# Kernel tuning notes

Hardware: AMD Instinct MI355X
Metric: run time of the kernel (lower is better)

Reference implementation:

```python
import jax, jax.numpy as jnp
import numpy as np
from jax import lax

B, N, C = 8, 1024, 768
H = 12          # num_heads
D = C // H      # head_dim = 64
CH = 2          # c_h head-mix group size
G = H // CH     # number of head groups = 6
CQ = CK = 3     # conv kernel sizes


def setup_inputs() -> dict:
    key = jax.random.key(0)
    ks = jax.random.split(key, 13)
    s = 0.02
    return {
        "query": jax.random.normal(ks[0], (B, N, C), jnp.float32),
        "key": jax.random.normal(ks[1], (B, N, C), jnp.float32),
        "value": jax.random.normal(ks[2], (B, N, C), jnp.float32),
        "Wq": jax.random.normal(ks[3], (C, C), jnp.float32) * s,
        "bq": jax.random.normal(ks[4], (C,), jnp.float32) * s,
        "Wk": jax.random.normal(ks[5], (C, C), jnp.float32) * s,
        "bk": jax.random.normal(ks[6], (C,), jnp.float32) * s,
        "Wv": jax.random.normal(ks[7], (C, C), jnp.float32) * s,
        "bv": jax.random.normal(ks[8], (C,), jnp.float32) * s,
        "conv_w": jax.random.normal(ks[9], (H, 1, CQ, CK), jnp.float32) * 0.2,  # depthwise OIHW
        "head_mix": jax.random.normal(ks[10], (G, CH, CH), jnp.float32) * 0.5
                    + jnp.broadcast_to(jnp.eye(CH, dtype=jnp.float32), (G, CH, CH)),
        "Wo": jax.random.normal(ks[11], (C, C), jnp.float32) * s,
        "bo": jax.random.normal(ks[12], (C,), jnp.float32) * s,
    }


def reference(query, key, value, Wq, bq, Wk, bk, Wv, bv, conv_w, head_mix, Wo, bo):
    # projections (torch Linear: x @ W.T + b), then split heads -> (B, H, N, D)
    Q = (query @ Wq.T + bq).reshape(B, N, H, D).transpose(0, 2, 1, 3)
    K = (key   @ Wk.T + bk).reshape(B, N, H, D).transpose(0, 2, 1, 3)
    V = (value @ Wv.T + bv).reshape(B, N, H, D).transpose(0, 2, 1, 3)

    # scores: (B, H, Nq, Nk)
    scores = jnp.einsum('bhqd,bhkd->bhqk', Q, K) / jnp.sqrt(jnp.float32(D))

    # depthwise conv over the (Nq, Nk) score plane, groups = num_heads
    conv_attn = lax.conv_general_dilated(
        scores, conv_w,
        window_strides=(1, 1),
        padding=((CQ // 2, CQ // 2), (CK // 2, CK // 2)),
        dimension_numbers=('NCHW', 'OIHW', 'NCHW'),
        feature_group_count=H,
    )

    attn = jax.nn.softmax(conv_attn, axis=-1)  # (B, H, Nq, Nk)

    # cross-head mixing within groups of c_h heads
    attn_g = attn.reshape(B, G, CH, N, N)
    mixed = jnp.einsum('bghij,ghk->bgkij', attn_g, head_mix).reshape(B, H, N, N)

    out = jnp.einsum('bhqk,bhkd->bhqd', mixed, V)          # (B, H, N, D)
    out = out.transpose(0, 2, 1, 3).reshape(B, N, C)       # merge heads
    return out @ Wo.T + bo
```

## Files before the change

### kernel.cpp

```cpp
#include <hip/hip_runtime.h>
#include <stdint.h>

#define B_ 8
#define N_ 1024
#define C_ 768
#define H_ 12
#define G_ 6
#define QBLK 64
#define KSTEP 64
#define NQT 16
#define NKS 16

typedef __attribute__((ext_vector_type(8))) short bf16x8;
typedef __attribute__((ext_vector_type(8))) unsigned short u16x8;
typedef __attribute__((ext_vector_type(4))) float f32x4;

__device__ __forceinline__ float bf2f(unsigned short u) {
  return __uint_as_float(((unsigned)u) << 16);
}
__device__ __forceinline__ unsigned short f2bf(float f) {
  __bf16 b = (__bf16)f;
  unsigned short u;
  __builtin_memcpy(&u, &b, 2);
  return u;
}
__device__ __forceinline__ void gload16(const void* g, void* l) {
  __builtin_amdgcn_global_load_lds(
      (const __attribute__((address_space(1))) unsigned int*)g,
      (__attribute__((address_space(3))) unsigned int*)l, 16, 0, 0);
}

__global__ __launch_bounds__(256) void cvtX(
    const float* __restrict__ q, const float* __restrict__ k,
    const float* __restrict__ v, unsigned short* __restrict__ dst) {
  const float* src = (blockIdx.y == 0) ? q : (blockIdx.y == 1) ? k : v;
  unsigned short* d = dst + (size_t)blockIdx.y * ((size_t)B_ * N_ * C_);
  const size_t idx = ((size_t)blockIdx.x * 256 + threadIdx.x) * 8;
  const float4 f0 = *(const float4*)(src + idx);
  const float4 f1 = *(const float4*)(src + idx + 4);
  u16x8 o;
  o[0] = f2bf(f0.x); o[1] = f2bf(f0.y); o[2] = f2bf(f0.z); o[3] = f2bf(f0.w);
  o[4] = f2bf(f1.x); o[5] = f2bf(f1.y); o[6] = f2bf(f1.z); o[7] = f2bf(f1.w);
  *(u16x8*)(d + idx) = o;
}

__global__ __launch_bounds__(256) void cvtW(
    const float* __restrict__ wq, const float* __restrict__ wk,
    const float* __restrict__ wv, const float* __restrict__ wo,
    unsigned short* __restrict__ dst) {
  const float* src = (blockIdx.y == 0)   ? wq
                     : (blockIdx.y == 1) ? wk
                     : (blockIdx.y == 2) ? wv
                                         : wo;
  unsigned short* d = dst + (size_t)blockIdx.y * ((size_t)C_ * C_);
  const size_t idx = ((size_t)blockIdx.x * 256 + threadIdx.x) * 8;
  const float4 f0 = *(const float4*)(src + idx);
  const float4 f1 = *(const float4*)(src + idx + 4);
  u16x8 o;
  o[0] = f2bf(f0.x); o[1] = f2bf(f0.y); o[2] = f2bf(f0.z); o[3] = f2bf(f0.w);
  o[4] = f2bf(f1.x); o[5] = f2bf(f1.y); o[6] = f2bf(f1.z); o[7] = f2bf(f1.w);
  *(u16x8*)(d + idx) = o;
}

template <int MODE>
__device__ __forceinline__ void gemm_bf16(
    const unsigned short* __restrict__ X, const unsigned short* __restrict__ W,
    const float* __restrict__ bias, void* __restrict__ out, int row0, int col0,
    unsigned short* __restrict__ As, unsigned short* __restrict__ Bs) {
  const int tid = threadIdx.x;
  const int wid = tid >> 6, lane = tid & 63;
  const int lr = lane & 15, lk = (lane >> 4) << 3;
  const int qrow = (lane >> 4) << 2;
  const int wr = (wid & 1) << 6, wc = (wid >> 1) << 6;
  const int srow = (wid << 4) + (lane >> 2);
  const int scol = (lane & 3) << 3;
  const unsigned short* gA0 = X + (size_t)(row0 + srow) * C_ + scol;
  const unsigned short* gA1 = X + (size_t)(row0 + 64 + srow) * C_ + scol;
  const unsigned short* gB0 = W + (size_t)(col0 + srow) * C_ + scol;
  const unsigned short* gB1 = W + (size_t)(col0 + 64 + srow) * C_ + scol;
  unsigned short* lA0 = As + (wid << 9);
  unsigned short* lA1 = As + 2048 + (wid << 9);
  unsigned short* lB0 = Bs + (wid << 9);
  unsigned short* lB1 = Bs + 2048 + (wid << 9);
  f32x4 acc[4][4] = {};
  for (int k0 = 0; k0 < C_; k0 += 32) {
    gload16(gA0 + k0, lA0);
    gload16(gA1 + k0, lA1);
    gload16(gB0 + k0, lB0);
    gload16(gB1 + k0, lB1);
    __syncthreads();
    bf16x8 af[4], bg[4];
#pragma unroll
    for (int m = 0; m < 4; ++m)
      af[m] = *(const bf16x8*)&As[(wr + (m << 4) + lr) * 32 + lk];
#pragma unroll
    for (int n = 0; n < 4; ++n)
      bg[n] = *(const bf16x8*)&Bs[(wc + (n << 4) + lr) * 32 + lk];
#pragma unroll
    for (int m = 0; m < 4; ++m)
#pragma unroll
      for (int n = 0; n < 4; ++n)
        acc[m][n] = __builtin_amdgcn_mfma_f32_16x16x32_bf16(af[m], bg[n],
                                                            acc[m][n], 0, 0, 0);
    __syncthreads();
  }
#pragma unroll
  for (int m = 0; m < 4; ++m) {
#pragma unroll
    for (int n = 0; n < 4; ++n) {
      const int colc = col0 + wc + (n << 4) + lr;
      const float bv = bias[colc];
      if (MODE == 2) {
        const int r0 = row0 + wr + (m << 4) + qrow;
        const int bb = r0 >> 10, nn0 = r0 & 1023;
        const int hh = colc >> 6, dd = colc & 63;
        ushort4 pk;
        pk.x = f2bf(acc[m][n][0] + bv);
        pk.y = f2bf(acc[m][n][1] + bv);
        pk.z = f2bf(acc[m][n][2] + bv);
        pk.w = f2bf(acc[m][n][3] + bv);
        *(ushort4*)&((unsigned short*)out)[(((size_t)(bb * H_ + hh) << 6) + dd)
                                               * 1024 + nn0] = pk;
      } else {
#pragma unroll
        for (int q = 0; q < 4; ++q) {
          const int r = row0 + wr + (m << 4) + qrow + q;
          const float v = acc[m][n][q] + bv;
          if (MODE == 0) {
            ((float*)out)[(size_t)r * C_ + colc] = v;
          } else {
            const int bb = r >> 10, nn = r & 1023;
            const int hh = colc >> 6, dd = colc & 63;
            ((unsigned short*)out)[(((size_t)(bb * H_ + hh) << 10) + nn) * 64 +
                                   dd] = f2bf(v);
          }
        }
      }
    }
  }
}

__global__ __launch_bounds__(256) void proj3(
    const unsigned short* __restrict__ Xb, const unsigned short* __restrict__ Wb,
    const float* __restrict__ bq, const float* __restrict__ bk,
    const float* __restrict__ bv, unsigned short* Qb, unsigned short* Kb,
    unsigned short* Vt) {
  __shared__ __align__(16) unsigned short As[128 * 32];
  __shared__ __align__(16) unsigned short Bs[128 * 32];
  const int wg = blockIdx.x;
  const int nid = (wg & 7) * 144 + (wg >> 3);
  const int x = nid % 6, y = (nid / 6) & 63, z = nid / 384;
  const unsigned short* X = Xb + (size_t)z * B_ * N_ * C_;
  const unsigned short* W = Wb + (size_t)z * C_ * C_;
  if (z == 0)
    gemm_bf16<1>(X, W, bq, Qb, y << 7, x << 7, As, Bs);
  else if (z == 1)
    gemm_bf16<1>(X, W, bk, Kb, y << 7, x << 7, As, Bs);
  else
    gemm_bf16<2>(X, W, bv, Vt, y << 7, x << 7, As, Bs);
}

__global__ __launch_bounds__(256) void oproj(
    const unsigned short* __restrict__ X, const unsigned short* __restrict__ Wb,
    const float* __restrict__ bo, float* __restrict__ out) {
  __shared__ __align__(16) unsigned short As[128 * 32];
  __shared__ __align__(16) unsigned short Bs[128 * 32];
  const int wg = blockIdx.x;
  const int nid = (wg & 7) * 48 + (wg >> 3);
  const int x = nid % 6, y = nid / 6;
  gemm_bf16<0>(X, Wb + (size_t)3 * C_ * C_, bo, out, y << 7, x << 7, As, Bs);
}

__global__ __launch_bounds__(256, 2) void fused_attn(
    const unsigned short* __restrict__ Qb, const unsigned short* __restrict__ Kb,
    const unsigned short* __restrict__ Vt, const float* __restrict__ cw,
    const float* __restrict__ hm, unsigned short* __restrict__ pvout) {
  __shared__ __align__(16) unsigned char smem[52800];
  unsigned short* QPt = (unsigned short*)(smem + 33280);
  float* lsum = (float*)(smem + 52288);
#define KBASE(hh) (smem + (size_t)(hh)*8448)
#define VBASE(hh) (smem + 16896 + (size_t)(hh)*8192)

  const int wg = blockIdx.x;
  const int nid = (wg & 7) * 96 + (wg >> 3);
  const int qt = nid & 15;
  const int bg = nid >> 4;
  const int g = bg % G_, bb = bg / G_;
  const int i0 = qt << 6;

  const int tid = threadIdx.x;
  const int wid = tid >> 6, lane = tid & 63;
  const int lr = lane & 15, lg = lane >> 4;
  const int lk = lg << 3;

  const int h = wid >> 1, mt = wid & 1;

  const size_t HSTR = (size_t)N_ * 64;
  const unsigned short* Qz = Qb + (size_t)(bb * H_ + 2 * g) * HSTR;
  const unsigned short* Kz = Kb + (size_t)(bb * H_ + 2 * g) * HSTR;
  const unsigned short* Vz = Vt + (size_t)(bb * H_ + 2 * g) * HSTR;

  const int krow = tid >> 2, kd0 = (tid & 3) << 4;
  const int kc0 = (tid & 3) << 1;
  const int k2r = 64 + (tid >> 3), k2d = (tid & 7) << 3;
  const int vd = tid >> 2, vc0 = (tid & 3) << 4;

  u16x8 kreg[4], vreg[4];
  u16x8 kreg2[2];

  {
    const int gj = -1 + krow;
#pragma unroll
    for (int hh = 0; hh < 2; ++hh) {
      u16x8 a = {}, b = {};
      if (gj >= 0) {
        a = *(const u16x8*)(Kz + hh * HSTR + (size_t)gj * 64 + kd0);
        b = *(const u16x8*)(Kz + hh * HSTR + (size_t)gj * 64 + kd0 + 8);
      }
      kreg[2 * hh] = a; kreg[2 * hh + 1] = b;
    }
    if (tid < 16) {
      const int gj2 = -1 + k2r;
#pragma unroll
      for (int hh = 0; hh < 2; ++hh)
        kreg2[hh] = *(const u16x8*)(Kz + hh * HSTR + (size_t)gj2 * 64 + k2d);
    }
#pragma unroll
    for (int hh = 0; hh < 2; ++hh)
#pragma unroll
      for (int hf = 0; hf < 2; ++hf)
        vreg[2 * hh + hf] =
            *(const u16x8*)(Vz + hh * HSTR + (size_t)vd * 1024 + vc0 + (hf << 3));
  }

  {
    const int r = tid >> 2, d0 = (tid & 3) << 4;
    const int gi = i0 - 1 + r;
#pragma unroll
    for (int hh = 0; hh < 2; ++hh) {
      u16x8 qa = {}, qb = {};
      if (gi >= 0 && gi < N_) {
        qa = *(const u16x8*)(Qz + hh * HSTR + (size_t)gi * 64 + d0);
        qb = *(const u16x8*)(Qz + hh * HSTR + (size_t)gi * 64 + d0 + 8);
      }
      *(u16x8*)&QPt[((size_t)(hh * 66 + r)) * 72 + d0] = qa;
      *(u16x8*)&QPt[((size_t)(hh * 66 + r)) * 72 + d0 + 8] = qb;
    }
    if (tid < 16) {
      const int r2 = 64 + (tid >> 3);
      const int d0h = (tid & 7) << 3;
      const int gi2 = i0 - 1 + r2;
#pragma unroll
      for (int hh = 0; hh < 2; ++hh) {
        u16x8 qv = {};
        if (gi2 < N_)
          qv = *(const u16x8*)(Qz + hh * HSTR + (size_t)gi2 * 64 + d0h);
        *(u16x8*)&QPt[((size_t)(hh * 66 + r2)) * 72 + d0h] = qv;
      }
    }
  }
  __syncthreads();

  bf16x8 qtf[2][3][2];
  {
    float wc3[3][3];
#pragma unroll
    for (int a = 0; a < 3; ++a)
#pragma unroll
      for (int c = 0; c < 3; ++c)
        wc3[a][c] = cw[(2 * g + h) * 9 + a * 3 + c] *
                    (0.125f * 1.4426950408889634f);
#pragma unroll
    for (int qs = 0; qs < 2; ++qs) {
      const int ribase = (mt << 5) + (qs << 4) + lr;
#pragma unroll
      for (int dh = 0; dh < 2; ++dh) {
        const u16x8 qa =
            *(const u16x8*)&QPt[((size_t)(h * 66 + ribase + 0)) * 72 +
                                (dh << 5) + lk];
        const u16x8 qb =
            *(const u16x8*)&QPt[((size_t)(h * 66 + ribase + 1)) * 72 +
                                (dh << 5) + lk];
        const u16x8 qc =
            *(const u16x8*)&QPt[((size_t)(h * 66 + ribase + 2)) * 72 +
                                (dh << 5) + lk];
#pragma unroll
        for (int c = 0; c < 3; ++c) {
#pragma unroll
          for (int e = 0; e < 8; ++e) {
            const float v = bf2f(qa[e]) * wc3[0][c] + bf2f(qb[e]) * wc3[1][c] +
                            bf2f(qc[e]) * wc3[2][c];
            qtf[qs][c][dh][e] = (short)f2bf(v);
          }
        }
      }
    }
  }

  unsigned short* PtW = &QPt[(size_t)wid * 2304];

  const unsigned char* kbB = KBASE(h) + lr * 128;
  int kofs[3][2];
#pragma unroll
  for (int c = 0; c < 3; ++c)
#pragma unroll
    for (int dh = 0; dh < 2; ++dh)
      kofs[c][dh] = (((((dh << 2) + lg) ^ ((lr + c) & 7)) << 4)) + c * 128;
  const unsigned char* vbB0 = VBASE(0) + lr * 128;
  const unsigned char* vbB1 = VBASE(1) + lr * 128;
  int vofs[2];
#pragma unroll
  for (int kj = 0; kj < 2; ++kj)
    vofs[kj] = ((((kj << 2) + lg) ^ (lr & 7)) << 4);

  float mreg[2] = {-3.0e38f, -3.0e38f};
  float lreg[2] = {0.f, 0.f};
  f32x4 acc[2][2][4] = {};

  for (int s = 0; s < NKS; ++s) {
    {
      unsigned char* kr0 = KBASE(0) + krow * 128;
      unsigned char* kr1 = KBASE(1) + krow * 128;
      const int ksw = krow & 7;
      *(u16x8*)(kr0 + ((kc0 ^ ksw) << 4)) = kreg[0];
      *(u16x8*)(kr0 + (((kc0 + 1) ^ ksw) << 4)) = kreg[1];
      *(u16x8*)(kr1 + ((kc0 ^ ksw) << 4)) = kreg[2];
      *(u16x8*)(kr1 + (((kc0 + 1) ^ ksw) << 4)) = kreg[3];
      if (tid < 16) {
        const int k2sw = k2r & 7, k2c = tid & 7;
        *(u16x8*)(KBASE(0) + k2r * 128 + ((k2c ^ k2sw) << 4)) = kreg2[0];
        *(u16x8*)(KBASE(1) + k2r * 128 + ((k2c ^ k2sw) << 4)) = kreg2[1];
      }
      unsigned char* vr0 = VBASE(0) + vd * 128;
      unsigned char* vr1 = VBASE(1) + vd * 128;
      const int vsw = vd & 7, vcc = (tid & 3) << 1;
      *(u16x8*)(vr0 + ((vcc ^ vsw) << 4)) = vreg[0];
      *(u16x8*)(vr0 + (((vcc + 1) ^ vsw) << 4)) = vreg[1];
      *(u16x8*)(vr1 + ((vcc ^ vsw) << 4)) = vreg[2];
      *(u16x8*)(vr1 + (((vcc + 1) ^ vsw) << 4)) = vreg[3];
    }
    __syncthreads();

    if (s + 1 < NKS) {
      const int j1 = (s + 1) << 6;
      const int gj = j1 - 1 + krow;
#pragma unroll
      for (int hh = 0; hh < 2; ++hh) {
        kreg[2 * hh] = *(const u16x8*)(Kz + hh * HSTR + (size_t)gj * 64 + kd0);
        kreg[2 * hh + 1] =
            *(const u16x8*)(Kz + hh * HSTR + (size_t)gj * 64 + kd0 + 8);
      }
      if (tid < 16) {
        const int gj2 = j1 - 1 + k2r;
#pragma unroll
        for (int hh = 0; hh < 2; ++hh) {
          u16x8 a = {};
          if (gj2 < N_)
            a = *(const u16x8*)(Kz + hh * HSTR + (size_t)gj2 * 64 + k2d);
          kreg2[hh] = a;
        }
      }
#pragma unroll
      for (int hh = 0; hh < 2; ++hh)
#pragma unroll
        for (int hf = 0; hf < 2; ++hf)
          vreg[2 * hh + hf] = *(const u16x8*)(Vz + hh * HSTR + (size_t)vd * 1024 +
                                              j1 + vc0 + (hf << 3));
    }

    f32x4 racc[2][4] = {};
    __builtin_amdgcn_s_setprio(1);
#pragma unroll
    for (int c = 0; c < 3; ++c) {
#pragma unroll
      for (int dh = 0; dh < 2; ++dh) {
#pragma unroll
        for (int nt = 0; nt < 4; ++nt) {
          const bf16x8 ak = *(const bf16x8*)(kbB + nt * 2048 + kofs[c][dh]);
          racc[0][nt] = __builtin_amdgcn_mfma_f32_16x16x32_bf16(
              ak, qtf[0][c][dh], racc[0][nt], 0, 0, 0);
          racc[1][nt] = __builtin_amdgcn_mfma_f32_16x16x32_bf16(
              ak, qtf[1][c][dh], racc[1][nt], 0, 0, 0);
        }
      }
    }
    __builtin_amdgcn_s_setprio(0);

    {
      float pmax[2];
#pragma unroll
      for (int qs = 0; qs < 2; ++qs) {
        float pm = fmaxf(fmaxf(racc[qs][0][0], racc[qs][0][1]),
                         fmaxf(racc[qs][0][2], racc[qs][0][3]));
#pragma unroll
        for (int nt = 1; nt < 4; ++nt)
          pm = fmaxf(pm, fmaxf(fmaxf(racc[qs][nt][0], racc[qs][nt][1]),
                               fmaxf(racc[qs][nt][2], racc[qs][nt][3])));
        pm = fmaxf(pm, __shfl_xor(pm, 16));
        pm = fmaxf(pm, __shfl_xor(pm, 32));
        pmax[qs] = pm;
      }
      if (__any((pmax[0] > mreg[0] + 8.f) || (pmax[1] > mreg[1] + 8.f))) {
#pragma unroll
        for (int qs = 0; qs < 2; ++qs) {
          const float mn = fmaxf(mreg[qs], pmax[qs]);
          const float alpha = exp2f(mreg[qs] - mn);
          mreg[qs] = mn;
          lreg[qs] *= alpha;
          float a4[4];
#pragma unroll
          for (int q = 0; q < 4; ++q)
            a4[q] = __shfl(alpha, (lg << 4) | ((lg << 2) + q));
#pragma unroll
          for (int k2 = 0; k2 < 2; ++k2)
#pragma unroll
            for (int nt = 0; nt < 4; ++nt)
#pragma unroll
              for (int q = 0; q < 4; ++q) acc[k2][qs][nt][q] *= a4[q];
        }
      }
#pragma unroll
      for (int qs = 0; qs < 2; ++qs) {
        float rs = 0.f;
#pragma unroll
        for (int nt = 0; nt < 4; ++nt)
#pragma unroll
          for (int q = 0; q < 4; ++q) {
            const float p = exp2f(racc[qs][nt][q] - mreg[qs]);
            racc[qs][nt][q] = p;
            rs += p;
          }
        rs += __shfl_xor(rs, 16);
        rs += __shfl_xor(rs, 32);
        lreg[qs] += rs;
#pragma unroll
        for (int nt = 0; nt < 4; ++nt) {
          ushort4 pw;
          pw.x = f2bf(racc[qs][nt][0]); pw.y = f2bf(racc[qs][nt][1]);
          pw.z = f2bf(racc[qs][nt][2]); pw.w = f2bf(racc[qs][nt][3]);
          *(ushort4*)&PtW[(size_t)qs * 1152 + (size_t)lr * 72 + (nt << 4) +
                          (lg << 2)] = pw;
        }
      }
    }

    {
      bf16x8 paf[2][2];
#pragma unroll
      for (int qs = 0; qs < 2; ++qs) {
        paf[qs][0] = *(const bf16x8*)&PtW[(size_t)qs * 1152 + (size_t)lr * 72 + lk];
        paf[qs][1] =
            *(const bf16x8*)&PtW[(size_t)qs * 1152 + (size_t)lr * 72 + 32 + lk];
      }
      __builtin_amdgcn_s_setprio(1);
#pragma unroll
      for (int kj = 0; kj < 2; ++kj)
#pragma unroll
        for (int nt = 0; nt < 4; ++nt) {
          const bf16x8 bva = *(const bf16x8*)(vbB0 + nt * 2048 + vofs[kj]);
          const bf16x8 bvb = *(const bf16x8*)(vbB1 + nt * 2048 + vofs[kj]);
#pragma unroll
          for (int qs = 0; qs < 2; ++qs) {
            acc[0][qs][nt] = __builtin_amdgcn_mfma_f32_16x16x32_bf16(
                paf[qs][kj], bva, acc[0][qs][nt], 0, 0, 0);
            acc[1][qs][nt] = __builtin_amdgcn_mfma_f32_16x16x32_bf16(
                paf[qs][kj], bvb, acc[1][qs][nt], 0, 0, 0);
          }
        }
      __builtin_amdgcn_s_setprio(0);
    }
    __syncthreads();
  }

  if (lg == 0) {
    lsum[h * 64 + (mt << 5) + lr] = lreg[0];
    lsum[h * 64 + (mt << 5) + 16 + lr] = lreg[1];
  }
  __syncthreads();

  const float mw0 = hm[(g * 2 + h) * 2 + 0];
  const float mw1 = hm[(g * 2 + h) * 2 + 1];
  float* Os = (float*)smem;
  if (h == 1) {
#pragma unroll
    for (int qs = 0; qs < 2; ++qs)
#pragma unroll
      for (int q = 0; q < 4; ++q) {
        const int row = (mt << 5) + (qs << 4) + (lg << 2) + q;
        const float f0 = mw0 / lsum[64 + row];
        const float f1 = mw1 / lsum[64 + row];
#pragma unroll
        for (int nt = 0; nt < 4; ++nt) {
          Os[(size_t)(0 * 64 + row) * 68 + (nt << 4) + lr] =
              acc[0][qs][nt][q] * f0;
          Os[(size_t)(1 * 64 + row) * 68 + (nt << 4) + lr] =
              acc[1][qs][nt][q] * f1;
        }
      }
  }
  __syncthreads();
  if (h == 0) {
#pragma unroll
    for (int qs = 0; qs < 2; ++qs)
#pragma unroll
      for (int q = 0; q < 4; ++q) {
        const int row = (mt << 5) + (qs << 4) + (lg << 2) + q;
        const int gi = i0 + row;
        const float f0 = mw0 / lsum[row];
        const float f1 = mw1 / lsum[row];
#pragma unroll
        for (int nt = 0; nt < 4; ++nt) {
          const float v0 = acc[0][qs][nt][q] * f0 +
                           Os[(size_t)(0 * 64 + row) * 68 + (nt << 4) + lr];
          const float v1 = acc[1][qs][nt][q] * f1 +
                           Os[(size_t)(1 * 64 + row) * 68 + (nt << 4) + lr];
          pvout[(size_t)(bb * N_ + gi) * C_ + (2 * g + 0) * 64 + (nt << 4) +
                lr] = f2bf(v0);
          pvout[(size_t)(bb * N_ + gi) * C_ + (2 * g + 1) * 64 + (nt << 4) +
                lr] = f2bf(v1);
        }
      }
  }
#undef KBASE
#undef VBASE
}

extern "C" void kernel_launch(void* const* d_in, const int* in_sizes, int n_in,
                              void* d_out, int out_size, void* d_ws, size_t ws_size,
                              hipStream_t stream) {
  const float* query = (const float*)d_in[0];
  const float* key   = (const float*)d_in[1];
  const float* value = (const float*)d_in[2];
  const float* Wq = (const float*)d_in[3];
  const float* bq = (const float*)d_in[4];
  const float* Wk = (const float*)d_in[5];
  const float* bk = (const float*)d_in[6];
  const float* Wv = (const float*)d_in[7];
  const float* bv = (const float*)d_in[8];
  const float* cw = (const float*)d_in[9];
  const float* hm = (const float*)d_in[10];
  const float* Wo = (const float*)d_in[11];
  const float* bo = (const float*)d_in[12];
  float* out = (float*)d_out;

  char* ws = (char*)d_ws;
  const size_t SZ_BF = (size_t)B_ * H_ * N_ * 64 * 2;
  unsigned short* Qb = (unsigned short*)ws;
  unsigned short* Kb = (unsigned short*)(ws + SZ_BF);
  unsigned short* Vt = (unsigned short*)(ws + 2 * SZ_BF);
  unsigned short* pvb = (unsigned short*)(ws + 3 * SZ_BF);
  unsigned short* Xb = (unsigned short*)(ws + 4 * SZ_BF);
  unsigned short* Wb = (unsigned short*)(ws + 7 * SZ_BF);

  const dim3 blk(256);
  cvtX<<<dim3(3072, 3), blk, 0, stream>>>(query, key, value, Xb);
  cvtW<<<dim3(288, 4), blk, 0, stream>>>(Wq, Wk, Wv, Wo, Wb);
  proj3<<<dim3(1152), blk, 0, stream>>>(Xb, Wb, bq, bk, bv, Qb, Kb, Vt);
  fused_attn<<<dim3(768), blk, 0, stream>>>(Qb, Kb, Vt, cw, hm, pvb);
  oproj<<<dim3(384), blk, 0, stream>>>(pvb, Wb, bo, out);
}
```

Before: 177.6 us.

## Merge conversion kernels, load Q rows directly, and shrink attention LDS footprint

Merges the two fp32-to-bf16 conversion kernels into one launch. In the attention kernel, the Q halo rows are read straight from global memory into registers, which removes the Q LDS staging buffer and one barrier. The P-tile scratch is reduced to a single 16-row slab per wave by doing the P·V MFMAs immediately after each q-subtile's softmax. Together these cut shared memory from about 52.8 KB to 43 KB, which could allow more resident blocks, at the cost of redundant global reads of overlapping Q rows and less batching of the PV MFMAs.

Result: slower. 203.6 us (+14.7%).

```diff
diff --git a/kernel.cpp b/kernel.cpp
--- a/kernel.cpp
+++ b/kernel.cpp
@@ -30,30 +30,28 @@
       (__attribute__((address_space(3))) unsigned int*)l, 16, 0, 0);
 }
 
-__global__ __launch_bounds__(256) void cvtX(
+__global__ __launch_bounds__(256) void cvtAll(
     const float* __restrict__ q, const float* __restrict__ k,
-    const float* __restrict__ v, unsigned short* __restrict__ dst) {
-  const float* src = (blockIdx.y == 0) ? q : (blockIdx.y == 1) ? k : v;
-  unsigned short* d = dst + (size_t)blockIdx.y * ((size_t)B_ * N_ * C_);
-  const size_t idx = ((size_t)blockIdx.x * 256 + threadIdx.x) * 8;
-  const float4 f0 = *(const float4*)(src + idx);
-  const float4 f1 = *(const float4*)(src + idx + 4);
-  u16x8 o;
-  o[0] = f2bf(f0.x); o[1] = f2bf(f0.y); o[2] = f2bf(f0.z); o[3] = f2bf(f0.w);
-  o[4] = f2bf(f1.x); o[5] = f2bf(f1.y); o[6] = f2bf(f1.z); o[7] = f2bf(f1.w);
-  *(u16x8*)(d + idx) = o;
-}
-
-__global__ __launch_bounds__(256) void cvtW(
-    const float* __restrict__ wq, const float* __restrict__ wk,
-    const float* __restrict__ wv, const float* __restrict__ wo,
-    unsigned short* __restrict__ dst) {
-  const float* src = (blockIdx.y == 0)   ? wq
-                     : (blockIdx.y == 1) ? wk
-                     : (blockIdx.y == 2) ? wv
-                                         : wo;
-  unsigned short* d = dst + (size_t)blockIdx.y * ((size_t)C_ * C_);
-  const size_t idx = ((size_t)blockIdx.x * 256 + threadIdx.x) * 8;
+    const float* __restrict__ v, const float* __restrict__ wq,
+    const float* __restrict__ wk, const float* __restrict__ wv,
+    const float* __restrict__ wo, unsigned short* __restrict__ Xb,
+    unsigned short* __restrict__ Wb) {
+  const int bi = blockIdx.x;
+  const float* src;
+  unsigned short* d;
+  size_t base;
+  if (bi < 9216) {
+    const int t = bi / 3072;
+    src = (t == 0) ? q : (t == 1) ? k : v;
+    d = Xb + (size_t)t * ((size_t)B_ * N_ * C_);
+    base = (size_t)(bi % 3072) * 2048;
+  } else {
+    const int t = (bi - 9216) / 288;
+    src = (t == 0) ? wq : (t == 1) ? wk : (t == 2) ? wv : wo;
+    d = Wb + (size_t)t * ((size_t)C_ * C_);
+    base = (size_t)((bi - 9216) % 288) * 2048;
+  }
+  const size_t idx = base + (size_t)threadIdx.x * 8;
   const float4 f0 = *(const float4*)(src + idx);
   const float4 f1 = *(const float4*)(src + idx + 4);
   u16x8 o;
@@ -175,9 +173,8 @@
     const unsigned short* __restrict__ Qb, const unsigned short* __restrict__ Kb,
     const unsigned short* __restrict__ Vt, const float* __restrict__ cw,
     const float* __restrict__ hm, unsigned short* __restrict__ pvout) {
-  __shared__ __align__(16) unsigned char smem[52800];
-  unsigned short* QPt = (unsigned short*)(smem + 33280);
-  float* lsum = (float*)(smem + 52288);
+  __shared__ __align__(16) unsigned char smem[43008];
+  float* lsum = (float*)(smem + 42496);
 #define KBASE(hh) (smem + (size_t)(hh)*8448)
 #define VBASE(hh) (smem + 16896 + (size_t)(hh)*8192)
 
@@ -233,34 +230,6 @@
             *(const u16x8*)(Vz + hh * HSTR + (size_t)vd * 1024 + vc0 + (hf << 3));
   }
 
-  {
-    const int r = tid >> 2, d0 = (tid & 3) << 4;
-    const int gi = i0 - 1 + r;
-#pragma unroll
-    for (int hh = 0; hh < 2; ++hh) {
-      u16x8 qa = {}, qb = {};
-      if (gi >= 0 && gi < N_) {
-        qa = *(const u16x8*)(Qz + hh * HSTR + (size_t)gi * 64 + d0);
-        qb = *(const u16x8*)(Qz + hh * HSTR + (size_t)gi * 64 + d0 + 8);
-      }
-      *(u16x8*)&QPt[((size_t)(hh * 66 + r)) * 72 + d0] = qa;
-      *(u16x8*)&QPt[((size_t)(hh * 66 + r)) * 72 + d0 + 8] = qb;
-    }
-    if (tid < 16) {
-      const int r2 = 64 + (tid >> 3);
-      const int d0h = (tid & 7) << 3;
-      const int gi2 = i0 - 1 + r2;
-#pragma unroll
-      for (int hh = 0; hh < 2; ++hh) {
-        u16x8 qv = {};
-        if (gi2 < N_)
-          qv = *(const u16x8*)(Qz + hh * HSTR + (size_t)gi2 * 64 + d0h);
-        *(u16x8*)&QPt[((size_t)(hh * 66 + r2)) * 72 + d0h] = qv;
-      }
-    }
-  }
-  __syncthreads();
-
   bf16x8 qtf[2][3][2];
   {
     float wc3[3][3];
@@ -273,31 +242,35 @@
 #pragma unroll
     for (int qs = 0; qs < 2; ++qs) {
       const int ribase = (mt << 5) + (qs << 4) + lr;
-#pragma unroll
-      for (int dh = 0; dh < 2; ++dh) {
-        const u16x8 qa =
-            *(const u16x8*)&QPt[((size_t)(h * 66 + ribase + 0)) * 72 +
-                                (dh << 5) + lk];
-        const u16x8 qb =
-            *(const u16x8*)&QPt[((size_t)(h * 66 + ribase + 1)) * 72 +
-                                (dh << 5) + lk];
-        const u16x8 qc =
-            *(const u16x8*)&QPt[((size_t)(h * 66 + ribase + 2)) * 72 +
-                                (dh << 5) + lk];
-#pragma unroll
-        for (int c = 0; c < 3; ++c) {
+      u16x8 qrows[3][2];
+#pragma unroll
+      for (int a = 0; a < 3; ++a) {
+        const int gi = i0 + ribase - 1 + a;
+        const bool ok = ((unsigned)gi < (unsigned)N_);
+#pragma unroll
+        for (int dh = 0; dh < 2; ++dh) {
+          u16x8 qv = {};
+          if (ok)
+            qv = *(const u16x8*)(Qz + h * HSTR + (size_t)gi * 64 + (dh << 5) + lk);
+          qrows[a][dh] = qv;
+        }
+      }
+#pragma unroll
+      for (int c = 0; c < 3; ++c)
+#pragma unroll
+        for (int dh = 0; dh < 2; ++dh)
 #pragma unroll
           for (int e = 0; e < 8; ++e) {
-            const float v = bf2f(qa[e]) * wc3[0][c] + bf2f(qb[e]) * wc3[1][c] +
-                            bf2f(qc[e]) * wc3[2][c];
+            const float v = bf2f(qrows[0][dh][e]) * wc3[0][c] +
+                            bf2f(qrows[1][dh][e]) * wc3[1][c] +
+                            bf2f(qrows[2][dh][e]) * wc3[2][c];
             qtf[qs][c][dh][e] = (short)f2bf(v);
           }
-        }
-      }
-    }
-  }
-
-  unsigned short* PtW = &QPt[(size_t)wid * 2304];
+    }
+  }
+
+  unsigned short* PtW =
+      (unsigned short*)(smem + 33280) + (size_t)wid * 1152;
 
   const unsigned char* kbB = KBASE(h) + lr * 128;
   int kofs[3][2];
@@ -438,36 +411,25 @@
           ushort4 pw;
           pw.x = f2bf(racc[qs][nt][0]); pw.y = f2bf(racc[qs][nt][1]);
           pw.z = f2bf(racc[qs][nt][2]); pw.w = f2bf(racc[qs][nt][3]);
-          *(ushort4*)&PtW[(size_t)qs * 1152 + (size_t)lr * 72 + (nt << 4) +
-                          (lg << 2)] = pw;
-        }
-      }
-    }
-
-    {
-      bf16x8 paf[2][2];
-#pragma unroll
-      for (int qs = 0; qs < 2; ++qs) {
-        paf[qs][0] = *(const bf16x8*)&PtW[(size_t)qs * 1152 + (size_t)lr * 72 + lk];
-        paf[qs][1] =
-            *(const bf16x8*)&PtW[(size_t)qs * 1152 + (size_t)lr * 72 + 32 + lk];
-      }
-      __builtin_amdgcn_s_setprio(1);
-#pragma unroll
-      for (int kj = 0; kj < 2; ++kj)
-#pragma unroll
-        for (int nt = 0; nt < 4; ++nt) {
-          const bf16x8 bva = *(const bf16x8*)(vbB0 + nt * 2048 + vofs[kj]);
-          const bf16x8 bvb = *(const bf16x8*)(vbB1 + nt * 2048 + vofs[kj]);
-#pragma unroll
-          for (int qs = 0; qs < 2; ++qs) {
+          *(ushort4*)&PtW[(size_t)lr * 72 + (nt << 4) + (lg << 2)] = pw;
+        }
+        bf16x8 paf[2];
+        paf[0] = *(const bf16x8*)&PtW[(size_t)lr * 72 + lk];
+        paf[1] = *(const bf16x8*)&PtW[(size_t)lr * 72 + 32 + lk];
+        __builtin_amdgcn_s_setprio(1);
+#pragma unroll
+        for (int kj = 0; kj < 2; ++kj)
+#pragma unroll
+          for (int nt = 0; nt < 4; ++nt) {
+            const bf16x8 bva = *(const bf16x8*)(vbB0 + nt * 2048 + vofs[kj]);
+            const bf16x8 bvb = *(const bf16x8*)(vbB1 + nt * 2048 + vofs[kj]);
             acc[0][qs][nt] = __builtin_amdgcn_mfma_f32_16x16x32_bf16(
-                paf[qs][kj], bva, acc[0][qs][nt], 0, 0, 0);
+                paf[kj], bva, acc[0][qs][nt], 0, 0, 0);
             acc[1][qs][nt] = __builtin_amdgcn_mfma_f32_16x16x32_bf16(
-                paf[qs][kj], bvb, acc[1][qs][nt], 0, 0, 0);
+                paf[kj], bvb, acc[1][qs][nt], 0, 0, 0);
           }
-        }
-      __builtin_amdgcn_s_setprio(0);
+        __builtin_amdgcn_s_setprio(0);
+      }
     }
     __syncthreads();
   }
@@ -553,8 +515,8 @@
   unsigned short* Wb = (unsigned short*)(ws + 7 * SZ_BF);
 
   const dim3 blk(256);
-  cvtX<<<dim3(3072, 3), blk, 0, stream>>>(query, key, value, Xb);
-  cvtW<<<dim3(288, 4), blk, 0, stream>>>(Wq, Wk, Wv, Wo, Wb);
+  cvtAll<<<dim3(10368), blk, 0, stream>>>(query, key, value, Wq, Wk, Wv, Wo, Xb,
+                                          Wb);
   proj3<<<dim3(1152), blk, 0, stream>>>(Xb, Wb, bq, bk, bv, Qb, Kb, Vt);
   fused_attn<<<dim3(768), blk, 0, stream>>>(Qb, Kb, Vt, cw, hm, pvb);
   oproj<<<dim3(384), blk, 0, stream>>>(pvb, Wb, bo, out);
```
